# Performance work log

Measured on AMD Instinct MI355X. Metric: run time of the kernel, lower is better.

Reference implementation:

```python
import math
import jax, jax.numpy as jnp
import numpy as np

NUM_HEADS = 8
C_HIDDEN = 32
C_Q = 64
C_KV = 64
INF = 1.0e9


def setup_inputs() -> dict:
    key = jax.random.key(0)
    ks = jax.random.split(key, 8)
    B, S, Q, KV = 1, 128, 256, 256
    H, D = NUM_HEADS, C_HIDDEN
    input_q = jax.random.normal(ks[0], (B, S, Q, C_Q), dtype=jnp.float32)
    input_kv = jax.random.normal(ks[1], (B, S, KV, C_KV), dtype=jnp.float32)
    mask = jnp.ones((B, S, 1, 1, KV), dtype=jnp.float32)
    bias = jax.random.normal(ks[2], (B, 1, H, Q, KV), dtype=jnp.float32)
    # Glorot-ish init for projections
    wq = jax.random.normal(ks[3], (C_Q, H * D), dtype=jnp.float32) * (1.0 / math.sqrt(C_Q))
    wk = jax.random.normal(ks[4], (C_KV, H * D), dtype=jnp.float32) * (1.0 / math.sqrt(C_KV))
    wv = jax.random.normal(ks[5], (C_KV, H * D), dtype=jnp.float32) * (1.0 / math.sqrt(C_KV))
    wo = jax.random.normal(ks[6], (H * D, C_Q), dtype=jnp.float32) * (1.0 / math.sqrt(H * D))
    bo = jnp.zeros((C_Q,), dtype=jnp.float32)
    return {"input_q": input_q, "input_kv": input_kv, "mask": mask, "bias": bias,
            "wq": wq, "wk": wk, "wv": wv, "wo": wo, "bo": bo}


def _split_heads(x):
    # [..., L, H*D] -> [..., H, L, D]
    *lead, L, HD = x.shape
    x = x.reshape(*lead, L, NUM_HEADS, C_HIDDEN)
    return jnp.swapaxes(x, -2, -3)


def reference(input_q, input_kv, mask, bias, wq, wk, wv, wo, bo):
    q = _split_heads(input_q @ wq)   # [B,S,H,Q,D]
    k = _split_heads(input_kv @ wk)  # [B,S,H,KV,D]
    v = _split_heads(input_kv @ wv)  # [B,S,H,KV,D]
    scaling = 1.0 / math.sqrt(C_HIDDEN)
    a = jnp.einsum("bshqd,bshkd->bshqk", q * scaling, k)
    a = a + (mask - 1.0) * INF + bias
    a = jax.nn.softmax(a, axis=-1)
    o = jnp.einsum("bshqk,bshkd->bshqd", a, v)
    o = jnp.swapaxes(o, -2, -3)  # [B,S,Q,H,D]
    o = o.reshape(o.shape[:-2] + (NUM_HEADS * C_HIDDEN,))
    return o @ wo + bo
```

## Files before the change

### kernel.cpp

```cpp
#include <hip/hip_runtime.h>

typedef __bf16 bf16_t;
typedef __bf16 bf16x4_t __attribute__((ext_vector_type(4)));
typedef __bf16 bf16x8 __attribute__((ext_vector_type(8)));
typedef float f32x4 __attribute__((ext_vector_type(4)));

#define NH 8
#define DH 32
#define QL 256
#define KL 256
#define CIN 64
#define HD 256

__device__ __forceinline__ bf16_t f2bf(float x) { return (bf16_t)x; }

__device__ __forceinline__ f32x4 mfma16(bf16x8 a, bf16x8 b, f32x4 c) {
    return __builtin_amdgcn_mfma_f32_16x16x32_bf16(a, b, c, 0, 0, 0);
}

__launch_bounds__(256, 2)
__global__ void proj_s(const float* __restrict__ Xq, const float* __restrict__ Xkv,
                       const float* __restrict__ Wq, const float* __restrict__ Wk,
                       const float* __restrict__ Wv, const float* __restrict__ Wo,
                       bf16_t* __restrict__ Qf, bf16_t* __restrict__ Kf,
                       bf16_t* __restrict__ Vf, bf16_t* __restrict__ WoF) {
    const int b = blockIdx.x;
    const int s = b & 127, which = b >> 7;
    const int tid = threadIdx.x, lane = tid & 63, w = tid >> 6;
    const int quad = lane >> 4, l16 = lane & 15;
    const f32x4 vzero = {0.f, 0.f, 0.f, 0.f};

    __shared__ __attribute__((aligned(16))) bf16_t sX[QL][72];
    __shared__ __attribute__((aligned(16))) bf16_t sT[4][2][32][40];

    const float* __restrict__ X = (which == 0) ? Xq : Xkv;
    const float* __restrict__ W = (which == 0) ? Wq : (which == 1 ? Wk : Wv);
    const float scale = (which == 0) ? 0.17677669529663687f : 1.0f;

#pragma unroll
    for (int it = 0; it < 16; ++it) {
        const int idx = it * 256 + tid;
        const int row = idx >> 4, c4 = (idx & 15) << 2;
        const f32x4 x4 = *(const f32x4*)&X[(s * QL + row) * CIN + c4];
#pragma unroll
        for (int j = 0; j < 4; ++j) sX[row][c4 + j] = f2bf(x4[j] * scale);
    }
    __syncthreads();

    if (which == 1 && s == 0 && WoF != nullptr) {
#pragma unroll
        for (int hh = 0; hh < 2; ++hh) {
            const int h = w * 2 + hh;
#pragma unroll
            for (int nt = 0; nt < 4; ++nt) {
                bf16x8 f;
#pragma unroll
                for (int j = 0; j < 8; ++j)
                    f[j] = f2bf(Wo[(h * DH + quad * 8 + j) * CIN + nt * 16 + l16]);
                *(bf16x8*)&WoF[(size_t)(h * 4 + nt) * 512 + lane * 8] = f;
            }
        }
    }

#pragma unroll 1
    for (int hh = 0; hh < 2; ++hh) {
        const int h = w * 2 + hh;
        bf16x8 bw[2][2];
#pragma unroll
        for (int nt = 0; nt < 2; ++nt)
#pragma unroll
            for (int ks = 0; ks < 2; ++ks) {
                bf16x8 f;
#pragma unroll
                for (int j = 0; j < 8; ++j)
                    f[j] = f2bf(W[(ks * 32 + quad * 8 + j) * HD + h * DH + nt * 16 + l16]);
                bw[nt][ks] = f;
            }
        const size_t base = (size_t)(s * NH + h) * 8192;

        if (which < 2) {
            bf16_t* __restrict__ Dst = which ? Kf : Qf;
#pragma unroll 2
            for (int mt = 0; mt < 16; ++mt) {
                const bf16x8 a0 = *(const bf16x8*)&sX[mt * 16 + l16][quad * 8];
                const bf16x8 a1 = *(const bf16x8*)&sX[mt * 16 + l16][32 + quad * 8];
                f32x4 c0 = vzero, c1 = vzero;
                c0 = mfma16(a0, bw[0][0], c0);
                c0 = mfma16(a1, bw[0][1], c0);
                c1 = mfma16(a0, bw[1][0], c1);
                c1 = mfma16(a1, bw[1][1], c1);
#pragma unroll
                for (int nt = 0; nt < 2; ++nt) {
                    const f32x4 c = nt ? c1 : c0;
#pragma unroll
                    for (int r = 0; r < 4; ++r)
                        sT[w][mt & 1][quad * 4 + r][nt * 16 + l16] = f2bf(c[r]);
                }
                const bf16x8 frag = *(const bf16x8*)&sT[w][mt & 1][l16][quad * 8];
                *(bf16x8*)&Dst[base + (size_t)mt * 512 + lane * 8] = frag;
            }
        } else {
#pragma unroll 2
            for (int cs = 0; cs < 8; ++cs) {
                bf16x8 a[2][2];
#pragma unroll
                for (int u = 0; u < 2; ++u) {
                    a[u][0] = *(const bf16x8*)&sX[cs * 32 + u * 16 + l16][quad * 8];
                    a[u][1] = *(const bf16x8*)&sX[cs * 32 + u * 16 + l16][32 + quad * 8];
                }
#pragma unroll
                for (int u = 0; u < 2; ++u)
#pragma unroll
                    for (int nth = 0; nth < 2; ++nth) {
                        f32x4 c = mfma16(a[u][0], bw[nth][0], vzero);
                        c = mfma16(a[u][1], bw[nth][1], c);
#pragma unroll
                        for (int r = 0; r < 4; ++r)
                            sT[w][cs & 1][nth * 16 + l16][u * 16 + quad * 4 + r] = f2bf(c[r]);
                    }
#pragma unroll
                for (int nt = 0; nt < 2; ++nt) {
                    const bf16x8 frag = *(const bf16x8*)&sT[w][cs & 1][nt * 16 + l16][quad * 8];
                    *(bf16x8*)&Vf[base + (size_t)(cs * 2 + nt) * 512 + lane * 8] = frag;
                }
            }
        }
    }
}

__launch_bounds__(256, 4)
__global__ void attn3(const float* __restrict__ Mask, const float* __restrict__ Bias,
                      const bf16_t* __restrict__ Qf, const bf16_t* __restrict__ Kf,
                      const bf16_t* __restrict__ Vf, bf16_t* __restrict__ Ows) {
    const int s = blockIdx.x, qt = blockIdx.y, h = blockIdx.z;
    const int tid = threadIdx.x, lane = tid & 63, w = tid >> 6;
    const int quad = lane >> 4, l16 = lane & 15;
    const f32x4 vzero = {0.f, 0.f, 0.f, 0.f};

    __shared__ __attribute__((aligned(16))) bf16_t sPT[4][16][136];

    const int tile = qt * 4 + w, q0 = tile * 16;
    const size_t base = (size_t)(s * NH + h) * 8192;

    const bf16x8 qfr = *(const bf16x8*)&Qf[base + (size_t)tile * 512 + lane * 8];

    f32x4 sv[16];
    const float* bbase = &Bias[(size_t)(h * QL + q0 + l16) * KL];
    const float* mbase = &Mask[s * KL];
#pragma unroll
    for (int ct = 0; ct < 16; ++ct) {
        const f32x4 b4 = *(const f32x4*)&bbase[ct * 16 + quad * 4];
        const f32x4 m4 = *(const f32x4*)&mbase[ct * 16 + quad * 4];
        sv[ct] = b4 + (m4 - 1.0f) * 1.0e9f;
    }
#pragma unroll
    for (int ct = 0; ct < 16; ++ct) {
        const bf16x8 ak = *(const bf16x8*)&Kf[base + ct * 512 + lane * 8];
        sv[ct] = mfma16(ak, qfr, sv[ct]);
    }
    float mx = -1e30f;
#pragma unroll
    for (int ct = 0; ct < 16; ++ct)
#pragma unroll
        for (int r = 0; r < 4; ++r) mx = fmaxf(mx, sv[ct][r]);
    mx = fmaxf(mx, __shfl_xor(mx, 16, 64));
    mx = fmaxf(mx, __shfl_xor(mx, 32, 64));
    float sum = 0.f;
#pragma unroll
    for (int ct = 0; ct < 16; ++ct)
#pragma unroll
        for (int r = 0; r < 4; ++r) {
            const float e = __expf(sv[ct][r] - mx);
            sv[ct][r] = e;
            sum += e;
        }
    sum += __shfl_xor(sum, 16, 64);
    sum += __shfl_xor(sum, 32, 64);
    const float rs = 1.0f / sum;

    f32x4 o0 = vzero, o1 = vzero;
#pragma unroll
    for (int c = 0; c < 2; ++c) {
#pragma unroll
        for (int cc = 0; cc < 8; ++cc) {
            const int ct = c * 8 + cc;
            bf16x4_t pv;
#pragma unroll
            for (int r = 0; r < 4; ++r) pv[r] = f2bf(sv[ct][r] * rs);
            *(bf16x4_t*)&sPT[w][l16][cc * 16 + quad * 4] = pv;
        }
#pragma unroll
        for (int ks = 0; ks < 4; ++ks) {
            const bf16x8 ap = *(const bf16x8*)&sPT[w][l16][ks * 32 + quad * 8];
            const int cs = c * 4 + ks;
            const bf16x8 bv0 = *(const bf16x8*)&Vf[base + (size_t)(cs * 2 + 0) * 512 + lane * 8];
            const bf16x8 bv1 = *(const bf16x8*)&Vf[base + (size_t)(cs * 2 + 1) * 512 + lane * 8];
            o0 = mfma16(ap, bv0, o0);
            o1 = mfma16(ap, bv1, o1);
        }
    }
    bf16_t* dst = &Ows[base + (size_t)tile * 512];
#pragma unroll
    for (int nt = 0; nt < 2; ++nt) {
        const f32x4 o = nt ? o1 : o0;
#pragma unroll
        for (int r = 0; r < 4; ++r)
            dst[(quad * 4 + r) * DH + nt * 16 + l16] = f2bf(o[r]);
    }
}

__launch_bounds__(64, 4)
__global__ void outproj3(const bf16_t* __restrict__ Ows, const bf16_t* __restrict__ WoF,
                         const float* __restrict__ Bo, float* __restrict__ Out) {
    const int b = blockIdx.x;
    const int s = b >> 4, tile = b & 15;
    const int lane = threadIdx.x & 63;
    const int quad = lane >> 4, l16 = lane & 15;
    const f32x4 vzero = {0.f, 0.f, 0.f, 0.f};

    f32x4 acc[4];
#pragma unroll
    for (int nt = 0; nt < 4; ++nt) acc[nt] = vzero;
#pragma unroll
    for (int h = 0; h < NH; ++h) {
        const bf16x8 a = *(const bf16x8*)&Ows[((size_t)(s * NH + h) * 16 + tile) * 512 +
                                              l16 * DH + quad * 8];
#pragma unroll
        for (int nt = 0; nt < 4; ++nt) {
            const bf16x8 bwo = *(const bf16x8*)&WoF[(size_t)(h * 4 + nt) * 512 + lane * 8];
            acc[nt] = mfma16(a, bwo, acc[nt]);
        }
    }
    const int mr0 = b * 16;
#pragma unroll
    for (int nt = 0; nt < 4; ++nt) {
        const float bo = Bo[nt * 16 + l16];
#pragma unroll
        for (int r = 0; r < 4; ++r)
            Out[(mr0 + quad * 4 + r) * CIN + nt * 16 + l16] = acc[nt][r] + bo;
    }
}

__launch_bounds__(256, 4)
__global__ void outproj2(const bf16_t* __restrict__ Ows, const float* __restrict__ Wo,
                         const float* __restrict__ Bo, float* __restrict__ Out) {
    const int tid = threadIdx.x, lane = tid & 63, w = tid >> 6;
    const int quad = lane >> 4, l16 = lane & 15;
    const int R = blockIdx.x * 128;
    const int s = R >> 8;

    __shared__ __attribute__((aligned(16))) bf16_t sWoT[CIN][HD + 8];
    __shared__ float sBo[CIN];

#pragma unroll
    for (int it = 0; it < 16; ++it) {
        const int idx = it * 256 + tid;
        const int kk = idx >> 4, c4 = (idx & 15) << 2;
        const f32x4 w4 = *(const f32x4*)&Wo[kk * CIN + c4];
#pragma unroll
        for (int j = 0; j < 4; ++j) sWoT[c4 + j][kk] = f2bf(w4[j]);
    }
    if (tid < CIN) sBo[tid] = Bo[tid];
    __syncthreads();

    const f32x4 vzero = {0.f, 0.f, 0.f, 0.f};
#pragma unroll 1
    for (int i = 0; i < 2; ++i) {
        const int mr0 = R + w * 32 + i * 16;
        const int tile = (mr0 & 255) >> 4;
        bf16x8 a[8];
#pragma unroll
        for (int ks = 0; ks < 8; ++ks)
            a[ks] = *(const bf16x8*)&Ows[((size_t)(s * NH + ks) * 16 + tile) * 512 +
                                         l16 * DH + quad * 8];
        f32x4 acc[4];
#pragma unroll
        for (int nt = 0; nt < 4; ++nt) acc[nt] = vzero;
#pragma unroll
        for (int ks = 0; ks < 8; ++ks)
#pragma unroll
            for (int nt = 0; nt < 4; ++nt) {
                const bf16x8 bb = *(const bf16x8*)&sWoT[nt * 16 + l16][ks * 32 + quad * 8];
                acc[nt] = mfma16(a[ks], bb, acc[nt]);
            }
#pragma unroll
        for (int nt = 0; nt < 4; ++nt) {
            const float bo = sBo[nt * 16 + l16];
#pragma unroll
            for (int r = 0; r < 4; ++r)
                Out[(mr0 + quad * 4 + r) * CIN + nt * 16 + l16] = acc[nt][r] + bo;
        }
    }
}

extern "C" void kernel_launch(void* const* d_in, const int* in_sizes, int n_in,
                              void* d_out, int out_size, void* d_ws, size_t ws_size,
                              hipStream_t stream) {
    const float* Xq   = (const float*)d_in[0];
    const float* Xkv  = (const float*)d_in[1];
    const float* Mask = (const float*)d_in[2];
    const float* Bias = (const float*)d_in[3];
    const float* Wq   = (const float*)d_in[4];
    const float* Wk   = (const float*)d_in[5];
    const float* Wv   = (const float*)d_in[6];
    const float* Wo   = (const float*)d_in[7];
    const float* Bo   = (const float*)d_in[8];
    float* Out = (float*)d_out;

    const size_t SEG = 16777216;
    bf16_t* Qf  = (bf16_t*)d_ws;
    bf16_t* Kf  = (bf16_t*)((char*)d_ws + SEG);
    bf16_t* Vf  = (bf16_t*)((char*)d_ws + 2 * SEG);
    bf16_t* Ows = Qf;
    const bool haveWoF = ws_size >= 3 * SEG + 32768;
    bf16_t* WoF = haveWoF ? (bf16_t*)((char*)d_ws + 3 * SEG) : nullptr;

    proj_s<<<384, 256, 0, stream>>>(Xq, Xkv, Wq, Wk, Wv, Wo, Qf, Kf, Vf, WoF);
    attn3<<<dim3(128, 4, NH), 256, 0, stream>>>(Mask, Bias, Qf, Kf, Vf, Ows);
    if (haveWoF)
        outproj3<<<2048, 64, 0, stream>>>(Ows, WoF, Bo, Out);
    else
        outproj2<<<256, 256, 0, stream>>>(Ows, Wo, Bo, Out);
}
```

Before: 151.8 us.

## Fuse QKV projection, attention and output projection into one kernel

Replaces the three-stage pipeline (projection kernel writing Q/K/V to workspace, attention kernel, output-projection kernel) with a small weight-packing kernel plus a single fused kernel. Each block handles one sequence and a quarter of the queries, recomputes K and V per head into shared memory, projects Q in registers, runs softmax attention, and accumulates the output projection across heads before writing the final result. This removes the global-memory round trips for Q, K, V and the per-head attention output, and two kernel launches. In exchange, K/V projection is redone by each of the 4 query-quarter blocks, and there are more block barriers per head.

Result: no change. 149.4 us (-1.6%).

```diff
diff --git a/kernel.cpp b/kernel.cpp
--- a/kernel.cpp
+++ b/kernel.cpp
@@ -18,54 +18,17 @@
     return __builtin_amdgcn_mfma_f32_16x16x32_bf16(a, b, c, 0, 0, 0);
 }
 
-__launch_bounds__(256, 2)
-__global__ void proj_s(const float* __restrict__ Xq, const float* __restrict__ Xkv,
-                       const float* __restrict__ Wq, const float* __restrict__ Wk,
+__launch_bounds__(256)
+__global__ void pack_w(const float* __restrict__ Wq, const float* __restrict__ Wk,
                        const float* __restrict__ Wv, const float* __restrict__ Wo,
-                       bf16_t* __restrict__ Qf, bf16_t* __restrict__ Kf,
-                       bf16_t* __restrict__ Vf, bf16_t* __restrict__ WoF) {
-    const int b = blockIdx.x;
-    const int s = b & 127, which = b >> 7;
+                       bf16_t* __restrict__ WqF, bf16_t* __restrict__ WkF,
+                       bf16_t* __restrict__ WvF, bf16_t* __restrict__ WoF) {
+    const int h = blockIdx.x;
     const int tid = threadIdx.x, lane = tid & 63, w = tid >> 6;
     const int quad = lane >> 4, l16 = lane & 15;
-    const f32x4 vzero = {0.f, 0.f, 0.f, 0.f};
-
-    __shared__ __attribute__((aligned(16))) bf16_t sX[QL][72];
-    __shared__ __attribute__((aligned(16))) bf16_t sT[4][2][32][40];
-
-    const float* __restrict__ X = (which == 0) ? Xq : Xkv;
-    const float* __restrict__ W = (which == 0) ? Wq : (which == 1 ? Wk : Wv);
-    const float scale = (which == 0) ? 0.17677669529663687f : 1.0f;
-
-#pragma unroll
-    for (int it = 0; it < 16; ++it) {
-        const int idx = it * 256 + tid;
-        const int row = idx >> 4, c4 = (idx & 15) << 2;
-        const f32x4 x4 = *(const f32x4*)&X[(s * QL + row) * CIN + c4];
-#pragma unroll
-        for (int j = 0; j < 4; ++j) sX[row][c4 + j] = f2bf(x4[j] * scale);
-    }
-    __syncthreads();
-
-    if (which == 1 && s == 0 && WoF != nullptr) {
-#pragma unroll
-        for (int hh = 0; hh < 2; ++hh) {
-            const int h = w * 2 + hh;
-#pragma unroll
-            for (int nt = 0; nt < 4; ++nt) {
-                bf16x8 f;
-#pragma unroll
-                for (int j = 0; j < 8; ++j)
-                    f[j] = f2bf(Wo[(h * DH + quad * 8 + j) * CIN + nt * 16 + l16]);
-                *(bf16x8*)&WoF[(size_t)(h * 4 + nt) * 512 + lane * 8] = f;
-            }
-        }
-    }
-
-#pragma unroll 1
-    for (int hh = 0; hh < 2; ++hh) {
-        const int h = w * 2 + hh;
-        bf16x8 bw[2][2];
+    if (w < 3) {
+        const float* __restrict__ W = (w == 0) ? Wq : (w == 1 ? Wk : Wv);
+        bf16_t* __restrict__ F = (w == 0) ? WqF : (w == 1 ? WkF : WvF);
 #pragma unroll
         for (int nt = 0; nt < 2; ++nt)
 #pragma unroll
@@ -74,222 +37,215 @@
 #pragma unroll
                 for (int j = 0; j < 8; ++j)
                     f[j] = f2bf(W[(ks * 32 + quad * 8 + j) * HD + h * DH + nt * 16 + l16]);
-                bw[nt][ks] = f;
-            }
-        const size_t base = (size_t)(s * NH + h) * 8192;
-
-        if (which < 2) {
-            bf16_t* __restrict__ Dst = which ? Kf : Qf;
-#pragma unroll 2
-            for (int mt = 0; mt < 16; ++mt) {
-                const bf16x8 a0 = *(const bf16x8*)&sX[mt * 16 + l16][quad * 8];
-                const bf16x8 a1 = *(const bf16x8*)&sX[mt * 16 + l16][32 + quad * 8];
-                f32x4 c0 = vzero, c1 = vzero;
-                c0 = mfma16(a0, bw[0][0], c0);
-                c0 = mfma16(a1, bw[0][1], c0);
-                c1 = mfma16(a0, bw[1][0], c1);
-                c1 = mfma16(a1, bw[1][1], c1);
-#pragma unroll
-                for (int nt = 0; nt < 2; ++nt) {
-                    const f32x4 c = nt ? c1 : c0;
-#pragma unroll
-                    for (int r = 0; r < 4; ++r)
-                        sT[w][mt & 1][quad * 4 + r][nt * 16 + l16] = f2bf(c[r]);
-                }
-                const bf16x8 frag = *(const bf16x8*)&sT[w][mt & 1][l16][quad * 8];
-                *(bf16x8*)&Dst[base + (size_t)mt * 512 + lane * 8] = frag;
-            }
-        } else {
-#pragma unroll 2
-            for (int cs = 0; cs < 8; ++cs) {
-                bf16x8 a[2][2];
-#pragma unroll
-                for (int u = 0; u < 2; ++u) {
-                    a[u][0] = *(const bf16x8*)&sX[cs * 32 + u * 16 + l16][quad * 8];
-                    a[u][1] = *(const bf16x8*)&sX[cs * 32 + u * 16 + l16][32 + quad * 8];
-                }
-#pragma unroll
-                for (int u = 0; u < 2; ++u)
-#pragma unroll
-                    for (int nth = 0; nth < 2; ++nth) {
-                        f32x4 c = mfma16(a[u][0], bw[nth][0], vzero);
-                        c = mfma16(a[u][1], bw[nth][1], c);
-#pragma unroll
-                        for (int r = 0; r < 4; ++r)
-                            sT[w][cs & 1][nth * 16 + l16][u * 16 + quad * 4 + r] = f2bf(c[r]);
-                    }
-#pragma unroll
-                for (int nt = 0; nt < 2; ++nt) {
-                    const bf16x8 frag = *(const bf16x8*)&sT[w][cs & 1][nt * 16 + l16][quad * 8];
-                    *(bf16x8*)&Vf[base + (size_t)(cs * 2 + nt) * 512 + lane * 8] = frag;
-                }
-            }
-        }
-    }
-}
-
-__launch_bounds__(256, 4)
-__global__ void attn3(const float* __restrict__ Mask, const float* __restrict__ Bias,
-                      const bf16_t* __restrict__ Qf, const bf16_t* __restrict__ Kf,
-                      const bf16_t* __restrict__ Vf, bf16_t* __restrict__ Ows) {
-    const int s = blockIdx.x, qt = blockIdx.y, h = blockIdx.z;
+                *(bf16x8*)&F[(size_t)((h * 4 + nt * 2 + ks) * 512) + lane * 8] = f;
+            }
+    } else {
+#pragma unroll
+        for (int nt = 0; nt < 4; ++nt) {
+            bf16x8 f;
+#pragma unroll
+            for (int j = 0; j < 8; ++j)
+                f[j] = f2bf(Wo[(h * DH + quad * 8 + j) * CIN + nt * 16 + l16]);
+            *(bf16x8*)&WoF[(size_t)((h * 4 + nt) * 512) + lane * 8] = f;
+        }
+    }
+}
+
+__launch_bounds__(256, 2)
+__global__ void fused_attn(const float* __restrict__ Xq, const float* __restrict__ Xkv,
+                           const float* __restrict__ Mask, const float* __restrict__ Bias,
+                           const bf16_t* __restrict__ WqF, const bf16_t* __restrict__ WkF,
+                           const bf16_t* __restrict__ WvF, const bf16_t* __restrict__ WoF,
+                           const float* __restrict__ Bo, float* __restrict__ Out) {
+    const int b = blockIdx.x;
+    const int s = b & 127, qq = b >> 7;
     const int tid = threadIdx.x, lane = tid & 63, w = tid >> 6;
     const int quad = lane >> 4, l16 = lane & 15;
+    const int tg = qq * 4 + w;
     const f32x4 vzero = {0.f, 0.f, 0.f, 0.f};
 
-    __shared__ __attribute__((aligned(16))) bf16_t sPT[4][16][136];
-
-    const int tile = qt * 4 + w, q0 = tile * 16;
-    const size_t base = (size_t)(s * NH + h) * 8192;
-
-    const bf16x8 qfr = *(const bf16x8*)&Qf[base + (size_t)tile * 512 + lane * 8];
-
-    f32x4 sv[16];
-    const float* bbase = &Bias[(size_t)(h * QL + q0 + l16) * KL];
-    const float* mbase = &Mask[s * KL];
-#pragma unroll
-    for (int ct = 0; ct < 16; ++ct) {
-        const f32x4 b4 = *(const f32x4*)&bbase[ct * 16 + quad * 4];
-        const f32x4 m4 = *(const f32x4*)&mbase[ct * 16 + quad * 4];
-        sv[ct] = b4 + (m4 - 1.0f) * 1.0e9f;
-    }
-#pragma unroll
-    for (int ct = 0; ct < 16; ++ct) {
-        const bf16x8 ak = *(const bf16x8*)&Kf[base + ct * 512 + lane * 8];
-        sv[ct] = mfma16(ak, qfr, sv[ct]);
-    }
-    float mx = -1e30f;
-#pragma unroll
-    for (int ct = 0; ct < 16; ++ct)
-#pragma unroll
-        for (int r = 0; r < 4; ++r) mx = fmaxf(mx, sv[ct][r]);
-    mx = fmaxf(mx, __shfl_xor(mx, 16, 64));
-    mx = fmaxf(mx, __shfl_xor(mx, 32, 64));
-    float sum = 0.f;
-#pragma unroll
-    for (int ct = 0; ct < 16; ++ct)
-#pragma unroll
-        for (int r = 0; r < 4; ++r) {
-            const float e = __expf(sv[ct][r] - mx);
-            sv[ct][r] = e;
-            sum += e;
-        }
-    sum += __shfl_xor(sum, 16, 64);
-    sum += __shfl_xor(sum, 32, 64);
-    const float rs = 1.0f / sum;
-
-    f32x4 o0 = vzero, o1 = vzero;
-#pragma unroll
-    for (int c = 0; c < 2; ++c) {
-#pragma unroll
-        for (int cc = 0; cc < 8; ++cc) {
-            const int ct = c * 8 + cc;
-            bf16x4_t pv;
-#pragma unroll
-            for (int r = 0; r < 4; ++r) pv[r] = f2bf(sv[ct][r] * rs);
-            *(bf16x4_t*)&sPT[w][l16][cc * 16 + quad * 4] = pv;
-        }
-#pragma unroll
-        for (int ks = 0; ks < 4; ++ks) {
-            const bf16x8 ap = *(const bf16x8*)&sPT[w][l16][ks * 32 + quad * 8];
-            const int cs = c * 4 + ks;
-            const bf16x8 bv0 = *(const bf16x8*)&Vf[base + (size_t)(cs * 2 + 0) * 512 + lane * 8];
-            const bf16x8 bv1 = *(const bf16x8*)&Vf[base + (size_t)(cs * 2 + 1) * 512 + lane * 8];
-            o0 = mfma16(ap, bv0, o0);
-            o1 = mfma16(ap, bv1, o1);
-        }
-    }
-    bf16_t* dst = &Ows[base + (size_t)tile * 512];
-#pragma unroll
-    for (int nt = 0; nt < 2; ++nt) {
-        const f32x4 o = nt ? o1 : o0;
-#pragma unroll
-        for (int r = 0; r < 4; ++r)
-            dst[(quad * 4 + r) * DH + nt * 16 + l16] = f2bf(o[r]);
-    }
-}
-
-__launch_bounds__(64, 4)
-__global__ void outproj3(const bf16_t* __restrict__ Ows, const bf16_t* __restrict__ WoF,
-                         const float* __restrict__ Bo, float* __restrict__ Out) {
-    const int b = blockIdx.x;
-    const int s = b >> 4, tile = b & 15;
-    const int lane = threadIdx.x & 63;
-    const int quad = lane >> 4, l16 = lane & 15;
-    const f32x4 vzero = {0.f, 0.f, 0.f, 0.f};
+    __shared__ __attribute__((aligned(16))) bf16_t sK[KL][40];
+    __shared__ __attribute__((aligned(16))) bf16_t sVT[DH][264];
+    __shared__ __attribute__((aligned(16))) bf16_t sB[4][16][136];
+    __shared__ __attribute__((aligned(16))) float sMask[KL];
+
+    if (tid < 64) {
+        const f32x4 m4 = *(const f32x4*)&Mask[s * KL + tid * 4];
+        f32x4 mm;
+#pragma unroll
+        for (int j = 0; j < 4; ++j) mm[j] = (m4[j] - 1.0f) * 1.0e9f;
+        *(f32x4*)&sMask[tid * 4] = mm;
+    }
+
+    bf16x8 xk[4][2];
+#pragma unroll
+    for (int t = 0; t < 4; ++t) {
+        const int row = (w * 4 + t) * 16 + l16;
+        const float* src = &Xkv[(size_t)(s * QL + row) * CIN];
+#pragma unroll
+        for (int ks = 0; ks < 2; ++ks) {
+            const f32x4 lo = *(const f32x4*)&src[ks * 32 + quad * 8];
+            const f32x4 hi = *(const f32x4*)&src[ks * 32 + quad * 8 + 4];
+            bf16x8 f;
+#pragma unroll
+            for (int j = 0; j < 4; ++j) { f[j] = f2bf(lo[j]); f[4 + j] = f2bf(hi[j]); }
+            xk[t][ks] = f;
+        }
+    }
+    bf16x8 xq[2];
+    {
+        const int row = tg * 16 + l16;
+        const float* src = &Xq[(size_t)(s * QL + row) * CIN];
+#pragma unroll
+        for (int ks = 0; ks < 2; ++ks) {
+            const f32x4 lo = *(const f32x4*)&src[ks * 32 + quad * 8];
+            const f32x4 hi = *(const f32x4*)&src[ks * 32 + quad * 8 + 4];
+            bf16x8 f;
+#pragma unroll
+            for (int j = 0; j < 4; ++j) {
+                f[j] = f2bf(lo[j] * 0.17677669529663687f);
+                f[4 + j] = f2bf(hi[j] * 0.17677669529663687f);
+            }
+            xq[ks] = f;
+        }
+    }
 
     f32x4 acc[4];
 #pragma unroll
     for (int nt = 0; nt < 4; ++nt) acc[nt] = vzero;
-#pragma unroll
+
+#pragma unroll 1
     for (int h = 0; h < NH; ++h) {
-        const bf16x8 a = *(const bf16x8*)&Ows[((size_t)(s * NH + h) * 16 + tile) * 512 +
-                                              l16 * DH + quad * 8];
-#pragma unroll
-        for (int nt = 0; nt < 4; ++nt) {
-            const bf16x8 bwo = *(const bf16x8*)&WoF[(size_t)(h * 4 + nt) * 512 + lane * 8];
-            acc[nt] = mfma16(a, bwo, acc[nt]);
-        }
-    }
-    const int mr0 = b * 16;
+        bf16x8 bk[2][2], bv[2][2];
+#pragma unroll
+        for (int nt = 0; nt < 2; ++nt)
+#pragma unroll
+            for (int ks = 0; ks < 2; ++ks) {
+                bk[nt][ks] = *(const bf16x8*)&WkF[(size_t)((h * 4 + nt * 2 + ks) * 512) + lane * 8];
+                bv[nt][ks] = *(const bf16x8*)&WvF[(size_t)((h * 4 + nt * 2 + ks) * 512) + lane * 8];
+            }
+#pragma unroll
+        for (int t = 0; t < 4; ++t) {
+            const int r0 = (w * 4 + t) * 16 + quad * 4;
+#pragma unroll
+            for (int nt = 0; nt < 2; ++nt) {
+                f32x4 c = mfma16(xk[t][0], bk[nt][0], vzero);
+                c = mfma16(xk[t][1], bk[nt][1], c);
+#pragma unroll
+                for (int r = 0; r < 4; ++r) sK[r0 + r][nt * 16 + l16] = f2bf(c[r]);
+            }
+        }
+        f32x4 sv[16];
+        const float* bb = &Bias[(size_t)(h * QL + tg * 16 + l16) * KL];
+#pragma unroll
+        for (int ct = 0; ct < 16; ++ct) sv[ct] = *(const f32x4*)&bb[ct * 16 + quad * 4];
+#pragma unroll
+        for (int t = 0; t < 4; ++t) {
+            const int c0 = (w * 4 + t) * 16 + quad * 4;
+#pragma unroll
+            for (int nt = 0; nt < 2; ++nt) {
+                f32x4 c = mfma16(xk[t][0], bv[nt][0], vzero);
+                c = mfma16(xk[t][1], bv[nt][1], c);
+                bf16x4_t p;
+#pragma unroll
+                for (int r = 0; r < 4; ++r) p[r] = f2bf(c[r]);
+                *(bf16x4_t*)&sVT[nt * 16 + l16][c0] = p;
+            }
+        }
+        {
+            bf16x8 bq[2][2];
+#pragma unroll
+            for (int nt = 0; nt < 2; ++nt)
+#pragma unroll
+                for (int ks = 0; ks < 2; ++ks)
+                    bq[nt][ks] = *(const bf16x8*)&WqF[(size_t)((h * 4 + nt * 2 + ks) * 512) + lane * 8];
+#pragma unroll
+            for (int nt = 0; nt < 2; ++nt) {
+                f32x4 c = mfma16(xq[0], bq[nt][0], vzero);
+                c = mfma16(xq[1], bq[nt][1], c);
+#pragma unroll
+                for (int r = 0; r < 4; ++r) sB[w][quad * 4 + r][nt * 16 + l16] = f2bf(c[r]);
+            }
+        }
+        const bf16x8 qfr = *(const bf16x8*)&sB[w][l16][quad * 8];
+
+        __syncthreads();
+
+#pragma unroll
+        for (int ct = 0; ct < 16; ++ct)
+            sv[ct] += *(const f32x4*)&sMask[ct * 16 + quad * 4];
+#pragma unroll
+        for (int ct = 0; ct < 16; ++ct) {
+            const bf16x8 ak = *(const bf16x8*)&sK[ct * 16 + l16][quad * 8];
+            sv[ct] = mfma16(ak, qfr, sv[ct]);
+        }
+        float mx = -1e30f;
+#pragma unroll
+        for (int ct = 0; ct < 16; ++ct)
+#pragma unroll
+            for (int r = 0; r < 4; ++r) mx = fmaxf(mx, sv[ct][r]);
+        mx = fmaxf(mx, __shfl_xor(mx, 16, 64));
+        mx = fmaxf(mx, __shfl_xor(mx, 32, 64));
+        float sum = 0.f;
+#pragma unroll
+        for (int ct = 0; ct < 16; ++ct)
+#pragma unroll
+            for (int r = 0; r < 4; ++r) {
+                const float e = __expf(sv[ct][r] - mx);
+                sv[ct][r] = e;
+                sum += e;
+            }
+        sum += __shfl_xor(sum, 16, 64);
+        sum += __shfl_xor(sum, 32, 64);
+        const float rs = 1.0f / sum;
+
+        f32x4 o0 = vzero, o1 = vzero;
+#pragma unroll
+        for (int c = 0; c < 2; ++c) {
+#pragma unroll
+            for (int cc = 0; cc < 8; ++cc) {
+                const int ct = c * 8 + cc;
+                bf16x4_t pv;
+#pragma unroll
+                for (int r = 0; r < 4; ++r) pv[r] = f2bf(sv[ct][r] * rs);
+                *(bf16x4_t*)&sB[w][l16][cc * 16 + quad * 4] = pv;
+            }
+#pragma unroll
+            for (int ks = 0; ks < 4; ++ks) {
+                const bf16x8 ap = *(const bf16x8*)&sB[w][l16][ks * 32 + quad * 8];
+                const int cs = c * 4 + ks;
+                const bf16x8 v0 = *(const bf16x8*)&sVT[l16][cs * 32 + quad * 8];
+                const bf16x8 v1 = *(const bf16x8*)&sVT[16 + l16][cs * 32 + quad * 8];
+                o0 = mfma16(ap, v0, o0);
+                o1 = mfma16(ap, v1, o1);
+            }
+        }
+
+        __syncthreads();
+
+        {
+            bf16x8 bwo[4];
+#pragma unroll
+            for (int nt = 0; nt < 4; ++nt)
+                bwo[nt] = *(const bf16x8*)&WoF[(size_t)((h * 4 + nt) * 512) + lane * 8];
+#pragma unroll
+            for (int r = 0; r < 4; ++r) {
+                sB[w][quad * 4 + r][l16] = f2bf(o0[r]);
+                sB[w][quad * 4 + r][16 + l16] = f2bf(o1[r]);
+            }
+            const bf16x8 af = *(const bf16x8*)&sB[w][l16][quad * 8];
+#pragma unroll
+            for (int nt = 0; nt < 4; ++nt) acc[nt] = mfma16(af, bwo[nt], acc[nt]);
+        }
+    }
+
+    const int orow = s * QL + tg * 16 + quad * 4;
 #pragma unroll
     for (int nt = 0; nt < 4; ++nt) {
         const float bo = Bo[nt * 16 + l16];
 #pragma unroll
         for (int r = 0; r < 4; ++r)
-            Out[(mr0 + quad * 4 + r) * CIN + nt * 16 + l16] = acc[nt][r] + bo;
-    }
-}
-
-__launch_bounds__(256, 4)
-__global__ void outproj2(const bf16_t* __restrict__ Ows, const float* __restrict__ Wo,
-                         const float* __restrict__ Bo, float* __restrict__ Out) {
-    const int tid = threadIdx.x, lane = tid & 63, w = tid >> 6;
-    const int quad = lane >> 4, l16 = lane & 15;
-    const int R = blockIdx.x * 128;
-    const int s = R >> 8;
-
-    __shared__ __attribute__((aligned(16))) bf16_t sWoT[CIN][HD + 8];
-    __shared__ float sBo[CIN];
-
-#pragma unroll
-    for (int it = 0; it < 16; ++it) {
-        const int idx = it * 256 + tid;
-        const int kk = idx >> 4, c4 = (idx & 15) << 2;
-        const f32x4 w4 = *(const f32x4*)&Wo[kk * CIN + c4];
-#pragma unroll
-        for (int j = 0; j < 4; ++j) sWoT[c4 + j][kk] = f2bf(w4[j]);
-    }
-    if (tid < CIN) sBo[tid] = Bo[tid];
-    __syncthreads();
-
-    const f32x4 vzero = {0.f, 0.f, 0.f, 0.f};
-#pragma unroll 1
-    for (int i = 0; i < 2; ++i) {
-        const int mr0 = R + w * 32 + i * 16;
-        const int tile = (mr0 & 255) >> 4;
-        bf16x8 a[8];
-#pragma unroll
-        for (int ks = 0; ks < 8; ++ks)
-            a[ks] = *(const bf16x8*)&Ows[((size_t)(s * NH + ks) * 16 + tile) * 512 +
-                                         l16 * DH + quad * 8];
-        f32x4 acc[4];
-#pragma unroll
-        for (int nt = 0; nt < 4; ++nt) acc[nt] = vzero;
-#pragma unroll
-        for (int ks = 0; ks < 8; ++ks)
-#pragma unroll
-            for (int nt = 0; nt < 4; ++nt) {
-                const bf16x8 bb = *(const bf16x8*)&sWoT[nt * 16 + l16][ks * 32 + quad * 8];
-                acc[nt] = mfma16(a[ks], bb, acc[nt]);
-            }
-#pragma unroll
-        for (int nt = 0; nt < 4; ++nt) {
-            const float bo = sBo[nt * 16 + l16];
-#pragma unroll
-            for (int r = 0; r < 4; ++r)
-                Out[(mr0 + quad * 4 + r) * CIN + nt * 16 + l16] = acc[nt][r] + bo;
-        }
+            Out[(size_t)(orow + r) * CIN + nt * 16 + l16] = acc[nt][r] + bo;
     }
 }
 
@@ -307,18 +263,12 @@
     const float* Bo   = (const float*)d_in[8];
     float* Out = (float*)d_out;
 
-    const size_t SEG = 16777216;
-    bf16_t* Qf  = (bf16_t*)d_ws;
-    bf16_t* Kf  = (bf16_t*)((char*)d_ws + SEG);
-    bf16_t* Vf  = (bf16_t*)((char*)d_ws + 2 * SEG);
-    bf16_t* Ows = Qf;
-    const bool haveWoF = ws_size >= 3 * SEG + 32768;
-    bf16_t* WoF = haveWoF ? (bf16_t*)((char*)d_ws + 3 * SEG) : nullptr;
-
-    proj_s<<<384, 256, 0, stream>>>(Xq, Xkv, Wq, Wk, Wv, Wo, Qf, Kf, Vf, WoF);
-    attn3<<<dim3(128, 4, NH), 256, 0, stream>>>(Mask, Bias, Qf, Kf, Vf, Ows);
-    if (haveWoF)
-        outproj3<<<2048, 64, 0, stream>>>(Ows, WoF, Bo, Out);
-    else
-        outproj2<<<256, 256, 0, stream>>>(Ows, Wo, Bo, Out);
-}
+    bf16_t* WqF = (bf16_t*)d_ws;
+    bf16_t* WkF = WqF + 16384;
+    bf16_t* WvF = WkF + 16384;
+    bf16_t* WoF = WvF + 16384;
+
+    pack_w<<<dim3(NH), 256, 0, stream>>>(Wq, Wk, Wv, Wo, WqF, WkF, WvF, WoF);
+    fused_attn<<<dim3(512), 256, 0, stream>>>(Xq, Xkv, Mask, Bias,
+                                              WqF, WkF, WvF, WoF, Bo, Out);
+}
```
